# Performance work log

Hardware: AMD Instinct MI355X
Metric: run time of the kernel (lower is better)

The kernel has to match this reference:

```python
import jax, jax.numpy as jnp
import numpy as np

EPS = 1e-5
NUM_GROUPS = 32


def setup_inputs() -> dict:
    key = jax.random.key(0)
    ks = jax.random.split(key, 4)
    B, C, H, W = 8, 128, 64, 64
    x = jax.random.normal(ks[0], (B, C, H, W), dtype=jnp.float32)
    gamma = jnp.ones((C,), dtype=jnp.float32)
    beta = jnp.zeros((C,), dtype=jnp.float32)
    # 1x1 convs stored as dense [out, in] matrices (kaiming-ish scale)
    w_qkv = jax.random.normal(ks[1], (3 * C, C), dtype=jnp.float32) * (1.0 / np.sqrt(C))
    b_qkv = jnp.zeros((3 * C,), dtype=jnp.float32)
    w_out = jax.random.normal(ks[2], (C, C), dtype=jnp.float32) * (1.0 / np.sqrt(C))
    b_out = jnp.zeros((C,), dtype=jnp.float32)
    return {"x": x, "gamma": gamma, "beta": beta, "w_qkv": w_qkv,
            "b_qkv": b_qkv, "w_out": w_out, "b_out": b_out}


def _group_norm(x, gamma, beta):
    B, C, H, W = x.shape
    xg = x.reshape(B, NUM_GROUPS, C // NUM_GROUPS, H, W)
    mean = jnp.mean(xg, axis=(2, 3, 4), keepdims=True)
    var = jnp.var(xg, axis=(2, 3, 4), keepdims=True)
    xn = ((xg - mean) * jax.lax.rsqrt(var + EPS)).reshape(B, C, H, W)
    return xn * gamma[None, :, None, None] + beta[None, :, None, None]


def reference(x, gamma, beta, w_qkv, b_qkv, w_out, b_out):
    B, C, H, W = x.shape
    hw = H * W
    xn = _group_norm(x, gamma, beta)
    # 1x1 conv C -> 3C
    qkv = jnp.einsum('oc,bchw->bohw', w_qkv, xn) + b_qkv[None, :, None, None]
    q, k, v = jnp.split(qkv, 3, axis=1)           # each [B, C, H, W]
    q = q.reshape(B, C, hw).transpose(0, 2, 1)    # [B, hw, C]
    k = k.reshape(B, C, hw)                       # [B, C, hw]
    v = v.reshape(B, C, hw).transpose(0, 2, 1)    # [B, hw, C]
    scale = C ** (-0.5)
    weights = jnp.einsum('bnc,bcm->bnm', q, k) * scale  # [B, hw, hw]
    attn = jax.nn.softmax(weights, axis=-1)
    out = jnp.einsum('bnm,bmc->bnc', attn, v)     # [B, hw, C]
    out = out.reshape(B, H, W, C).transpose(0, 3, 1, 2)  # [B, C, H, W]
    out = jnp.einsum('oc,bchw->bohw', w_out, out) + b_out[None, :, None, None]
    return out + x
```

## Files before the change

kernel.cpp:

```cpp
#include <hip/hip_runtime.h>

typedef __attribute__((ext_vector_type(8))) short short8;
typedef __attribute__((ext_vector_type(4))) float f32x4;
typedef unsigned short u16;
typedef unsigned int u32;

__device__ __forceinline__ float bf2f(u16 h) {
  union { u32 u; float f; } c; c.u = ((u32)h) << 16; return c.f;
}
__device__ __forceinline__ u16 f2bf(float f) {
  union { float f; u32 u; } c; c.f = f;
  u32 u = c.u;
  u32 r = u + 0x7fffu + ((u >> 16) & 1u);
  return (u16)(r >> 16);
}
__device__ __forceinline__ u16 f2bf_fast(float f) {
  union { float f; u32 u; } c; c.f = f;
  return (u16)((c.u + 0x8000u) >> 16);
}
__device__ __forceinline__ f32x4 mfma16(short8 a, short8 b, f32x4 c) {
  return __builtin_amdgcn_mfma_f32_16x16x32_bf16(a, b, c, 0, 0, 0);
}
__device__ __forceinline__ void gl2lds(const u16* g, u16* l) {
  __builtin_amdgcn_global_load_lds(
      (const __attribute__((address_space(1))) void*)g,
      (__attribute__((address_space(3))) void*)l, 16, 0, 0);
}

__device__ __forceinline__ bool bf_mode(const void* gamma) {
  return ((const u16*)gamma)[0] == 0x3F80u;
}
__device__ __forceinline__ void load8(const void* p, size_t idx, bool isbf,
                                      float* o) {
  if (isbf) {
    const u16* q = (const u16*)p + idx;
    uint4 v = *(const uint4*)q;
    u32 w[4] = {v.x, v.y, v.z, v.w};
#pragma unroll
    for (int j = 0; j < 4; ++j) {
      o[2 * j]     = bf2f((u16)(w[j] & 0xffffu));
      o[2 * j + 1] = bf2f((u16)(w[j] >> 16));
    }
  } else {
    const float* q = (const float*)p + idx;
    float4 a = *(const float4*)q;
    float4 b = *(const float4*)(q + 4);
    o[0] = a.x; o[1] = a.y; o[2] = a.z; o[3] = a.w;
    o[4] = b.x; o[5] = b.y; o[6] = b.z; o[7] = b.w;
  }
}
__device__ __forceinline__ float ldf(const void* p, size_t i, bool isbf) {
  return isbf ? bf2f(((const u16*)p)[i]) : ((const float*)p)[i];
}

__global__ __launch_bounds__(256) void stats_kernel(
    const void* __restrict__ x, const void* __restrict__ gamma,
    const void* __restrict__ w_qkv, const void* __restrict__ w_out,
    u16* __restrict__ w_bf, float* __restrict__ stats) {
  bool isbf = bf_mode(gamma);
  int bg = blockIdx.x;
  if (!isbf) {
    int i = bg * 256 + threadIdx.x;
    float v = (i < 49152) ? ((const float*)w_qkv)[i]
                          : ((const float*)w_out)[i - 49152];
    w_bf[i] = f2bf(v);
  }
  int b = bg >> 5, g = bg & 31;
  size_t base = ((size_t)b * 128 + g * 4) << 12;
  float s = 0.f, ss = 0.f;
  for (int i = threadIdx.x; i < 2048; i += 256) {
    float v[8];
    load8(x, base + (size_t)i * 8, isbf, v);
#pragma unroll
    for (int j = 0; j < 8; ++j) { s += v[j]; ss += v[j] * v[j]; }
  }
#pragma unroll
  for (int off = 32; off; off >>= 1) {
    s += __shfl_xor(s, off);
    ss += __shfl_xor(ss, off);
  }
  __shared__ float red[8];
  int wv = threadIdx.x >> 6, lane = threadIdx.x & 63;
  if (lane == 0) { red[wv] = s; red[4 + wv] = ss; }
  __syncthreads();
  if (threadIdx.x == 0) {
    float st = red[0] + red[1] + red[2] + red[3];
    float sst = red[4] + red[5] + red[6] + red[7];
    float mean = st * (1.f / 16384.f);
    float var = sst * (1.f / 16384.f) - mean * mean;
    stats[bg * 2] = mean;
    stats[bg * 2 + 1] = rsqrtf(var + 1e-5f);
  }
}

__global__ __launch_bounds__(256) void qkv_fused_kernel(
    const void* __restrict__ x, const float* __restrict__ stats,
    const void* __restrict__ gamma, const void* __restrict__ beta,
    const void* __restrict__ w_qkv_in, const void* __restrict__ b_qkv,
    const u16* __restrict__ w_bf, u16* __restrict__ Qt,
    u16* __restrict__ Kt_bfm, u16* __restrict__ Kt_fpm,
    u16* __restrict__ V) {
  bool isbf = bf_mode(gamma);
  const u16* wq = isbf ? (const u16*)w_qkv_in : w_bf;
  u16* Kt = isbf ? Kt_bfm : Kt_fpm;
  int nt = blockIdx.x, b = blockIdx.y;
  int n0 = nt * 64;
  int t = threadIdx.x;
  __shared__ __align__(16) u16 shb[9216];
  u16* xn = shb;
  {
    int cg = t >> 3, ng = t & 7;
    float mean = stats[(b * 32 + cg) * 2];
    float rstd = stats[(b * 32 + cg) * 2 + 1];
    float vals[4][8];
#pragma unroll
    for (int cc = 0; cc < 4; ++cc) {
      int c = cg * 4 + cc;
      float sc = ldf(gamma, c, isbf) * rstd;
      float sh = ldf(beta, c, isbf) - mean * sc;
      float v[8];
      load8(x, (((size_t)b * 128 + c) << 12) + n0 + ng * 8, isbf, v);
#pragma unroll
      for (int j = 0; j < 8; ++j) vals[cc][j] = v[j] * sc + sh;
    }
#pragma unroll
    for (int j = 0; j < 8; ++j) {
      ushort4 o;
      o.x = f2bf(vals[0][j]);
      o.y = f2bf(vals[1][j]);
      o.z = f2bf(vals[2][j]);
      o.w = f2bf(vals[3][j]);
      *(ushort4*)(xn + (ng * 8 + j) * 136 + cg * 4) = o;
    }
  }
  __syncthreads();
  int wv = t >> 6, lane = t & 63, l15 = lane & 15, quad = lane >> 4;
  short8 bfr[4][4];
#pragma unroll
  for (int mt = 0; mt < 4; ++mt)
#pragma unroll
    for (int kk = 0; kk < 4; ++kk)
      bfr[mt][kk] = *(const short8*)(xn + (mt * 16 + l15) * 136 + kk * 32 + quad * 8);
  __syncthreads();

  u16* res = shb;
#pragma unroll
  for (int g = 0; g < 3; ++g) {
#pragma unroll
    for (int rd = 0; rd < 2; ++rd) {
      int tl = rd * 4 + wv;
      int otg = g * 8 + tl;
      short8 a[4];
#pragma unroll
      for (int kk = 0; kk < 4; ++kk)
        a[kk] = *(const short8*)(wq + (size_t)(otg * 16 + l15) * 128 + kk * 32 + quad * 8);
      int o0 = otg * 16 + quad * 4;
      float bias[4];
#pragma unroll
      for (int r = 0; r < 4; ++r) bias[r] = ldf(b_qkv, o0 + r, isbf);
      int c0 = tl * 16 + quad * 4;
#pragma unroll
      for (int mt = 0; mt < 4; ++mt) {
        f32x4 acc = (f32x4){0.f, 0.f, 0.f, 0.f};
#pragma unroll
        for (int kk = 0; kk < 4; ++kk) acc = mfma16(a[kk], bfr[mt][kk], acc);
        int nl = mt * 16 + l15;
        if (g < 2) {
          ushort4 o;
          o.x = f2bf(acc[0] + bias[0]);
          o.y = f2bf(acc[1] + bias[1]);
          o.z = f2bf(acc[2] + bias[2]);
          o.w = f2bf(acc[3] + bias[3]);
          *(ushort4*)(res + nl * 136 + c0) = o;
        } else {
#pragma unroll
          for (int r = 0; r < 4; ++r)
            res[(c0 + r) * 72 + nl] = f2bf(acc[r] + bias[r]);
        }
      }
    }
    __syncthreads();
    if (g < 2) {
      int n = t >> 2, seg = t & 3;
      const uint4* src = (const uint4*)(res + n * 136 + seg * 32);
      uint4* dst = (uint4*)((g == 0 ? Qt : Kt) +
                            ((size_t)b * 4096 + n0 + n) * 128 + seg * 32);
#pragma unroll
      for (int i = 0; i < 4; ++i) dst[i] = src[i];
    } else {
      int c = t >> 1, hf = t & 1;
      const uint4* src = (const uint4*)(res + c * 72 + hf * 32);
      uint4* dst = (uint4*)(V + ((size_t)b * 128 + c) * 4096 + n0 + hf * 32);
#pragma unroll
      for (int i = 0; i < 4; ++i) dst[i] = src[i];
    }
    __syncthreads();
  }
}

__global__ __launch_bounds__(512, 1) void flash_kernel(
    const u16* __restrict__ Qt, const u16* __restrict__ Kt_bfm,
    const u16* __restrict__ Kt_fpm, const u16* __restrict__ V,
    u16* __restrict__ attn, const void* __restrict__ gamma, int fuse,
    const void* __restrict__ w_out_in, const u16* __restrict__ w_bf_out,
    const void* __restrict__ b_out, const void* __restrict__ x,
    void* __restrict__ out) {
  bool isbf = bf_mode(gamma);
  const u16* Kt = isbf ? Kt_bfm : Kt_fpm;
  int b = blockIdx.x, qt = blockIdx.y;
  int t = threadIdx.x;
  int wv = t >> 6, lane = t & 63;
  int l15 = lane & 15, quad = lane >> 4;
  int rset = wv >> 1, h = wv & 1;
  __shared__ __align__(16) u16 smem[32768];
  u16* kb0 = smem;
  u16* vb = smem + 16384;
  u16* pw = smem + 24576 + wv * 1024;
  const u16* Kb = Kt + (size_t)b * 4096 * 128;
  const u16* Vg = V + (size_t)b * 128 * 4096;

#pragma unroll
  for (int i2 = 0; i2 < 2; ++i2) {
    int i = wv * 2 + i2;
    int R = i * 4 + (lane >> 4);
    gl2lds(Kb + (size_t)R * 128 + (((lane & 15) ^ (R & 15)) << 3),
           &kb0[i * 512]);
  }

  int wq = qt * 128 + rset * 32;
  const float qs = 0.12753251f;
  const float M = 10.0f;
  short8 qf[2][4];
#pragma unroll
  for (int rs = 0; rs < 2; ++rs)
#pragma unroll
    for (int kk = 0; kk < 4; ++kk) {
      short8 raw = *(const short8*)(
          Qt + ((size_t)b * 4096 + wq + rs * 16 + l15) * 128 + kk * 32 + quad * 8);
      short8 o;
#pragma unroll
      for (int j = 0; j < 8; ++j) o[j] = (short)f2bf(bf2f((u16)raw[j]) * qs);
      qf[rs][kk] = o;
    }

  float lsum[2][4];
  f32x4 acc[2][8];
#pragma unroll
  for (int rs = 0; rs < 2; ++rs) {
#pragma unroll
    for (int r = 0; r < 4; ++r) lsum[rs][r] = 0.f;
#pragma unroll
    for (int ct = 0; ct < 8; ++ct) acc[rs][ct] = (f32x4){0.f, 0.f, 0.f, 0.f};
  }
  __syncthreads();

  for (int kt = 0; kt < 64; ++kt) {
    int s = kt & 1;
    int m0 = kt * 64;
    u16* kbs = kb0 + s * 8192;
#pragma unroll
    for (int i2 = 0; i2 < 2; ++i2) {
      int i = wv * 2 + i2;
      int c = i * 8 + (lane >> 3);
      gl2lds(Vg + (size_t)c * 4096 + m0 + (((lane & 7) ^ (c & 7)) << 3),
             &vb[i * 512]);
    }
    f32x4 sacc[2][2];
#pragma unroll
    for (int rs = 0; rs < 2; ++rs)
#pragma unroll
      for (int mt = 0; mt < 2; ++mt) sacc[rs][mt] = (f32x4){0.f, 0.f, 0.f, 0.f};
#pragma unroll
    for (int mt = 0; mt < 2; ++mt) {
      int R = h * 32 + mt * 16 + l15;
      short8 kf[4];
#pragma unroll
      for (int kk = 0; kk < 4; ++kk)
        kf[kk] = *(const short8*)(&kbs[R * 128 + (((kk * 4 + quad) ^ l15) << 3)]);
#pragma unroll
      for (int rs = 0; rs < 2; ++rs)
#pragma unroll
        for (int kk = 0; kk < 4; ++kk)
          sacc[rs][mt] = mfma16(qf[rs][kk], kf[kk], sacc[rs][mt]);
    }
#pragma unroll
    for (int rs = 0; rs < 2; ++rs)
#pragma unroll
      for (int mt = 0; mt < 2; ++mt)
#pragma unroll
        for (int r = 0; r < 4; ++r) {
          float p = __builtin_amdgcn_exp2f(sacc[rs][mt][r] - M);
          lsum[rs][r] += p;
          int row = rs * 16 + quad * 4 + r;
          int m = mt * 16 + l15;
          int msw = (((((m >> 3) ^ ((row >> 2) & 3)) & 3)) << 3) | (m & 7);
          pw[row * 32 + msw] = f2bf_fast(p);
        }
    __syncthreads();
    if (kt < 63) {
      int m1 = (kt + 1) * 64;
#pragma unroll
      for (int i2 = 0; i2 < 2; ++i2) {
        int i = wv * 2 + i2;
        int R = i * 4 + (lane >> 4);
        gl2lds(Kb + (size_t)(m1 + R) * 128 + (((lane & 15) ^ (R & 15)) << 3),
               &kb0[(s ^ 1) * 8192 + i * 512]);
      }
    }
    short8 pa[2];
#pragma unroll
    for (int rs = 0; rs < 2; ++rs) {
      int row = rs * 16 + l15;
      int ch = (quad ^ ((row >> 2) & 3)) & 3;
      pa[rs] = *(const short8*)(&pw[row * 32 + ch * 8]);
    }
#pragma unroll
    for (int ct = 0; ct < 8; ++ct) {
      int c = ct * 16 + l15;
      int ch = ((h * 4 + quad) ^ (c & 7)) & 7;
      short8 vbf = *(const short8*)(&vb[c * 64 + ch * 8]);
      acc[0][ct] = mfma16(pa[0], vbf, acc[0][ct]);
      acc[1][ct] = mfma16(pa[1], vbf, acc[1][ct]);
    }
    __syncthreads();
  }

  if (!fuse) {
    float* ef = (float*)smem;
#pragma unroll
    for (int rs = 0; rs < 2; ++rs) {
      if (h) {
#pragma unroll
        for (int ct = 0; ct < 8; ++ct)
          *(f32x4*)&ef[((rset * 8 + ct) * 64 + lane) * 4] = acc[rs][ct];
        if (rs == 0) {
#pragma unroll
          for (int j = 0; j < 8; ++j)
            ef[8192 + (rset * 64 + lane) * 8 + j] = lsum[j >> 2][j & 3];
        }
      }
      __syncthreads();
      if (!h) {
#pragma unroll
        for (int ct = 0; ct < 8; ++ct) {
          f32x4 o = *(const f32x4*)&ef[((rset * 8 + ct) * 64 + lane) * 4];
          acc[rs][ct] += o;
        }
        if (rs == 0) {
#pragma unroll
          for (int j = 0; j < 8; ++j)
            lsum[j >> 2][j & 3] += ef[8192 + (rset * 64 + lane) * 8 + j];
        }
      }
      __syncthreads();
    }
    if (!h) {
#pragma unroll
      for (int rs = 0; rs < 2; ++rs)
#pragma unroll
        for (int r = 0; r < 4; ++r) {
          float v = lsum[rs][r];
#pragma unroll
          for (int off = 1; off < 16; off <<= 1) v += __shfl_xor(v, off);
          lsum[rs][r] = 1.f / v;
        }
#pragma unroll
      for (int rs = 0; rs < 2; ++rs)
#pragma unroll
        for (int ct = 0; ct < 8; ++ct)
#pragma unroll
          for (int r = 0; r < 4; ++r) {
            int n = wq + rs * 16 + quad * 4 + r;
            attn[((size_t)b * 4096 + n) * 128 + ct * 16 + l15] =
                f2bf(acc[rs][ct][r] * lsum[rs][r]);
          }
    }
    return;
  }

  const u16* wo = isbf ? (const u16*)w_out_in : w_bf_out;
  int o_row = wv * 16;
  int o0 = o_row + quad * 4;
  int nbase = qt * 128;
  float xres[8][4];
#pragma unroll
  for (int nt16 = 0; nt16 < 8; ++nt16)
#pragma unroll
    for (int r = 0; r < 4; ++r) {
      size_t idx = ((size_t)b * 128 + o0 + r) * 4096 + nbase + nt16 * 16 + l15;
      xres[nt16][r] = ldf(x, idx, isbf);
    }
  short8 wa[4];
#pragma unroll
  for (int kk = 0; kk < 4; ++kk)
    wa[kk] = *(const short8*)(wo + (size_t)(o_row + l15) * 128 + kk * 32 + quad * 8);

  u16* Otile = smem;
  float* mrg = (float*)(smem + 17408);
  float* lmr = (float*)(smem + 25600);
  if (h) {
#pragma unroll
    for (int j = 0; j < 8; ++j)
      lmr[(rset * 64 + lane) * 8 + j] = lsum[j >> 2][j & 3];
  }
  __syncthreads();
  if (!h) {
#pragma unroll
    for (int rs = 0; rs < 2; ++rs)
#pragma unroll
      for (int r = 0; r < 4; ++r) {
        float v = lsum[rs][r] + lmr[(rset * 64 + lane) * 8 + rs * 4 + r];
#pragma unroll
        for (int off = 1; off < 16; off <<= 1) v += __shfl_xor(v, off);
        lsum[rs][r] = 1.f / v;
      }
  }
  __syncthreads();
#pragma unroll
  for (int rs = 0; rs < 2; ++rs)
#pragma unroll
    for (int cg2 = 0; cg2 < 2; ++cg2) {
      if (h) {
#pragma unroll
        for (int c4 = 0; c4 < 4; ++c4)
          *(f32x4*)&mrg[((rset * 4 + c4) * 64 + lane) * 4] = acc[rs][cg2 * 4 + c4];
      }
      __syncthreads();
      if (!h) {
#pragma unroll
        for (int c4 = 0; c4 < 4; ++c4) {
          int ct = cg2 * 4 + c4;
          f32x4 o = *(const f32x4*)&mrg[((rset * 4 + c4) * 64 + lane) * 4];
          int nloc = rset * 32 + rs * 16 + quad * 4;
#pragma unroll
          for (int r = 0; r < 4; ++r)
            Otile[(nloc + r) * 136 + ct * 16 + l15] =
                f2bf((acc[rs][ct][r] + o[r]) * lsum[rs][r]);
        }
      }
      __syncthreads();
    }
  f32x4 acc2[8];
#pragma unroll
  for (int nt16 = 0; nt16 < 8; ++nt16) {
    acc2[nt16] = (f32x4){0.f, 0.f, 0.f, 0.f};
#pragma unroll
    for (int kk = 0; kk < 4; ++kk) {
      short8 bfrag = *(const short8*)(
          &Otile[(nt16 * 16 + l15) * 136 + kk * 32 + quad * 8]);
      acc2[nt16] = mfma16(wa[kk], bfrag, acc2[nt16]);
    }
  }
  float bias[4];
#pragma unroll
  for (int r = 0; r < 4; ++r) bias[r] = ldf(b_out, o0 + r, isbf);
#pragma unroll
  for (int nt16 = 0; nt16 < 8; ++nt16) {
#pragma unroll
    for (int r = 0; r < 4; ++r) {
      size_t idx = ((size_t)b * 128 + o0 + r) * 4096 + nbase + nt16 * 16 + l15;
      float val = acc2[nt16][r] + bias[r] + xres[nt16][r];
      if (isbf) ((u16*)out)[idx] = f2bf(val);
      else      ((float*)out)[idx] = val;
    }
  }
}

__global__ __launch_bounds__(256) void proj_kernel(
    const u16* __restrict__ attn, const void* __restrict__ w_out_in,
    const u16* __restrict__ w_bf_out, const void* __restrict__ b_out,
    const void* __restrict__ x, const void* __restrict__ gamma,
    void* __restrict__ out) {
  bool isbf = bf_mode(gamma);
  const u16* wo = isbf ? (const u16*)w_out_in : w_bf_out;
  int nt = blockIdx.x, ot = blockIdx.y, b = blockIdx.z;
  int wv = threadIdx.x >> 6, lane = threadIdx.x & 63;
  int l15 = lane & 15, quad = lane >> 4;
  int o_row = ot * 64 + wv * 16;
  short8 a[4];
#pragma unroll
  for (int kk = 0; kk < 4; ++kk)
    a[kk] = *(const short8*)(wo + (size_t)(o_row + l15) * 128 + kk * 32 + quad * 8);
  const u16* bbase = attn + ((size_t)b * 4096 + nt * 64) * 128;
  f32x4 acc[4];
#pragma unroll
  for (int mt = 0; mt < 4; ++mt) {
    acc[mt] = (f32x4){0.f, 0.f, 0.f, 0.f};
#pragma unroll
    for (int kk = 0; kk < 4; ++kk) {
      short8 bf = *(const short8*)(bbase + (size_t)(mt * 16 + l15) * 128 + kk * 32 + quad * 8);
      acc[mt] = mfma16(a[kk], bf, acc[mt]);
    }
  }
  int o0 = o_row + quad * 4;
  float bias[4];
#pragma unroll
  for (int r = 0; r < 4; ++r) bias[r] = ldf(b_out, o0 + r, isbf);
#pragma unroll
  for (int mt = 0; mt < 4; ++mt) {
    int n = nt * 64 + mt * 16 + l15;
#pragma unroll
    for (int r = 0; r < 4; ++r) {
      size_t idx = ((size_t)b * 128 + o0 + r) * 4096 + n;
      float val = acc[mt][r] + bias[r] + ldf(x, idx, isbf);
      if (isbf) ((u16*)out)[idx] = f2bf(val);
      else      ((float*)out)[idx] = val;
    }
  }
}

__global__ __launch_bounds__(256) void copy_kernel(
    const void* __restrict__ x, const void* __restrict__ gamma,
    void* __restrict__ out, int n) {
  bool isbf = bf_mode(gamma);
  int i = blockIdx.x * 256 + threadIdx.x;
  if (i < n) {
    if (isbf) ((u16*)out)[i] = ((const u16*)x)[i];
    else      ((float*)out)[i] = ((const float*)x)[i];
  }
}

extern "C" void kernel_launch(void* const* d_in, const int* in_sizes, int n_in,
                              void* d_out, int out_size, void* d_ws, size_t ws_size,
                              hipStream_t stream) {
  (void)in_sizes; (void)n_in;
  const void* x     = d_in[0];
  const void* gamma = d_in[1];
  const void* beta  = d_in[2];
  const void* w_qkv = d_in[3];
  const void* b_qkv = d_in[4];
  const void* w_out = d_in[5];
  const void* b_out = d_in[6];
  char* ws = (char*)d_ws;

  const size_t MB = 1u << 20;
  const size_t need = 16 * MB + 4096;
  if (ws_size < need) {
    copy_kernel<<<dim3((out_size + 255) / 256), dim3(256), 0, stream>>>(
        x, gamma, d_out, out_size);
    return;
  }
  int fuse = (ws_size >= 24 * MB + 262144) ? 1 : 0;
  u16 *Qt, *Kt_bfm, *Kt_fpm, *Vb, *w_bf, *attn;
  float* stats;
  if (fuse) {
    Qt     = (u16*)ws;
    Kt_bfm = (u16*)(ws + 8 * MB);
    Kt_fpm = Kt_bfm;
    Vb     = (u16*)(ws + 16 * MB);
    stats  = (float*)(ws + 24 * MB);
    w_bf   = (u16*)(ws + 24 * MB + 4096);
    attn   = Qt;
  } else {
    Qt     = (u16*)ws;
    Kt_bfm = (u16*)(ws + 8 * MB);
    w_bf   = (u16*)(ws + 8 * MB + 4096);
    stats  = (float*)(ws + 16 * MB);
    Vb     = (u16*)d_out;
    Kt_fpm = (u16*)d_out + 4194304;
    attn   = Qt;
  }

  stats_kernel<<<dim3(256), dim3(256), 0, stream>>>(
      x, gamma, w_qkv, w_out, w_bf, stats);
  qkv_fused_kernel<<<dim3(64, 8), dim3(256), 0, stream>>>(
      x, stats, gamma, beta, w_qkv, b_qkv, w_bf, Qt, Kt_bfm, Kt_fpm, Vb);
  flash_kernel<<<dim3(8, 32), dim3(512), 0, stream>>>(
      Qt, Kt_bfm, Kt_fpm, Vb, attn, gamma, fuse,
      w_out, w_bf + 49152, b_out, x, d_out);
  if (!fuse)
    proj_kernel<<<dim3(64, 2, 8), dim3(256), 0, stream>>>(
        attn, w_out, w_bf + 49152, b_out, x, gamma, d_out);
}
```

Measured before the change: 190.2 us.

## Double-buffer V tiles and replace syncthreads with vmcnt-counted barriers

```diff
diff --git a/kernel.cpp b/kernel.cpp
--- a/kernel.cpp
+++ b/kernel.cpp
@@ -26,6 +26,9 @@
       (const __attribute__((address_space(1))) void*)g,
       (__attribute__((address_space(3))) void*)l, 16, 0, 0);
 }
+
+#define WAIT_BAR(N) \
+  asm volatile("s_waitcnt vmcnt(" #N ")\n\ts_barrier" ::: "memory")
 
 __device__ __forceinline__ bool bf_mode(const void* gamma) {
   return ((const u16*)gamma)[0] == 0x3F80u;
@@ -212,20 +215,33 @@
   int wv = t >> 6, lane = t & 63;
   int l15 = lane & 15, quad = lane >> 4;
   int rset = wv >> 1, h = wv & 1;
-  __shared__ __align__(16) u16 smem[32768];
+  __shared__ __align__(16) u16 smem[40960];
   u16* kb0 = smem;
-  u16* vb = smem + 16384;
-  u16* pw = smem + 24576 + wv * 1024;
+  u16* vb0 = smem + 16384;
+  u16* pw = smem + 32768 + wv * 1024;
   const u16* Kb = Kt + (size_t)b * 4096 * 128;
   const u16* Vg = V + (size_t)b * 128 * 4096;
 
-#pragma unroll
-  for (int i2 = 0; i2 < 2; ++i2) {
-    int i = wv * 2 + i2;
-    int R = i * 4 + (lane >> 4);
-    gl2lds(Kb + (size_t)R * 128 + (((lane & 15) ^ (R & 15)) << 3),
-           &kb0[i * 512]);
-  }
+  auto issueK = [&](int tile, u16* dst) {
+    int m = tile * 64;
+#pragma unroll
+    for (int i2 = 0; i2 < 2; ++i2) {
+      int i = wv * 2 + i2;
+      int R = i * 4 + (lane >> 4);
+      gl2lds(Kb + (size_t)(m + R) * 128 + (((lane & 15) ^ (R & 15)) << 3),
+             dst + i * 512);
+    }
+  };
+  auto issueV = [&](int tile, u16* dst) {
+    int m = tile * 64;
+#pragma unroll
+    for (int i2 = 0; i2 < 2; ++i2) {
+      int i = wv * 2 + i2;
+      int c = i * 8 + (lane >> 3);
+      gl2lds(Vg + (size_t)c * 4096 + m + (((lane & 7) ^ (c & 7)) << 3),
+             dst + i * 512);
+    }
+  };
 
   int wq = qt * 128 + rset * 32;
   const float qs = 0.12753251f;
@@ -242,6 +258,11 @@
       for (int j = 0; j < 8; ++j) o[j] = (short)f2bf(bf2f((u16)raw[j]) * qs);
       qf[rs][kk] = o;
     }
+  asm volatile("s_waitcnt vmcnt(0)" ::: "memory");
+
+  issueK(0, kb0);
+  issueV(0, vb0);
+  issueK(1, kb0 + 8192);
 
   float lsum[2][4];
   f32x4 acc[2][8];
@@ -252,19 +273,13 @@
 #pragma unroll
     for (int ct = 0; ct < 8; ++ct) acc[rs][ct] = (f32x4){0.f, 0.f, 0.f, 0.f};
   }
-  __syncthreads();
 
   for (int kt = 0; kt < 64; ++kt) {
     int s = kt & 1;
-    int m0 = kt * 64;
     u16* kbs = kb0 + s * 8192;
-#pragma unroll
-    for (int i2 = 0; i2 < 2; ++i2) {
-      int i = wv * 2 + i2;
-      int c = i * 8 + (lane >> 3);
-      gl2lds(Vg + (size_t)c * 4096 + m0 + (((lane & 7) ^ (c & 7)) << 3),
-             &vb[i * 512]);
-    }
+    u16* vbs = vb0 + s * 8192;
+    if (kt < 63) { WAIT_BAR(4); } else { WAIT_BAR(2); }
+    if (kt < 63) issueV(kt + 1, vb0 + (s ^ 1) * 8192);
     f32x4 sacc[2][2];
 #pragma unroll
     for (int rs = 0; rs < 2; ++rs)
@@ -296,17 +311,8 @@
           int msw = (((((m >> 3) ^ ((row >> 2) & 3)) & 3)) << 3) | (m & 7);
           pw[row * 32 + msw] = f2bf_fast(p);
         }
-    __syncthreads();
-    if (kt < 63) {
-      int m1 = (kt + 1) * 64;
-#pragma unroll
-      for (int i2 = 0; i2 < 2; ++i2) {
-        int i = wv * 2 + i2;
-        int R = i * 4 + (lane >> 4);
-        gl2lds(Kb + (size_t)(m1 + R) * 128 + (((lane & 15) ^ (R & 15)) << 3),
-               &kb0[(s ^ 1) * 8192 + i * 512]);
-      }
-    }
+    if (kt < 63) { WAIT_BAR(4); } else { WAIT_BAR(0); }
+    if (kt < 62) issueK(kt + 2, kbs);
     short8 pa[2];
 #pragma unroll
     for (int rs = 0; rs < 2; ++rs) {
@@ -318,12 +324,12 @@
     for (int ct = 0; ct < 8; ++ct) {
       int c = ct * 16 + l15;
       int ch = ((h * 4 + quad) ^ (c & 7)) & 7;
-      short8 vbf = *(const short8*)(&vb[c * 64 + ch * 8]);
+      short8 vbf = *(const short8*)(&vbs[c * 64 + ch * 8]);
       acc[0][ct] = mfma16(pa[0], vbf, acc[0][ct]);
       acc[1][ct] = mfma16(pa[1], vbf, acc[1][ct]);
     }
-    __syncthreads();
-  }
+  }
+  __syncthreads();
 
   if (!fuse) {
     float* ef = (float*)smem;
```

New measurement: 191.3 us. Within noise of the previous version (+0.6%).
